# Kernel optimization log

Measured on AMD Instinct MI355X. Metric: run time of the kernel, lower is better.

## Reference

```python
import jax, jax.numpy as jnp
import numpy as np


def setup_inputs() -> dict:
    key = jax.random.key(0)
    x = jax.random.normal(key, (16, 2048, 512), dtype=jnp.float32)
    return {"x": x}


def reference(x):
    # Cosine (L2-normalized) self-attention.
    # norm: [B, N, 1] L2 norm over feature dim
    norm = jnp.sqrt(jnp.sum(x * x, axis=2, keepdims=True))
    # scores[b, i, j] = <x_i, x_j> / (|x_i| |x_j|)  -> [B, N, N]
    scores = jnp.einsum('bnd,bmd->bnm', x, x) / (norm * jnp.swapaxes(norm, -2, -1))
    p_attn = jax.nn.softmax(scores, axis=-1)
    # output: [B, N, D]
    return jnp.einsum('bnm,bmd->bnd', p_attn, x)
```

## Files before the change

kernel.cpp:

```cpp
#include <hip/hip_runtime.h>
#include <hip/hip_bf16.h>
#include <cstdint>
#include <cstddef>

#define BB 16
#define NN 2048
#define DD 512

typedef _Float16 f16x8 __attribute__((ext_vector_type(8)));
typedef _Float16 f16x4 __attribute__((ext_vector_type(4)));
typedef float f32x4 __attribute__((ext_vector_type(4)));

__device__ __forceinline__ void async_ld16(void* lds, const void* g) {
    __builtin_amdgcn_global_load_lds(
        (const __attribute__((address_space(1))) unsigned int*)(uintptr_t)g,
        (__attribute__((address_space(3))) unsigned int*)(uint32_t)(uintptr_t)lds,
        16, 0, 0);
}

#define VM_WAIT(n) asm volatile("s_waitcnt vmcnt(" #n ")" ::: "memory")
#define RAW_BAR()  do { asm volatile("" ::: "memory"); __builtin_amdgcn_s_barrier(); asm volatile("" ::: "memory"); } while (0)
#define LGKM_BAR() do { asm volatile("s_waitcnt lgkmcnt(0)" ::: "memory"); \
                        __builtin_amdgcn_s_barrier();                      \
                        __builtin_amdgcn_sched_barrier(0); } while (0)

__global__ __launch_bounds__(256) void k_prep(const float* __restrict__ x,
                                              _Float16* __restrict__ xhn,
                                              _Float16* __restrict__ vT,
                                              float* __restrict__ denom) {
    __shared__ _Float16 t[512 * 66];
    const int tid = threadIdx.x, lane = tid & 63, w = tid >> 6;
    const int b = blockIdx.y, j0 = blockIdx.x * 64;
    if (tid < 64) denom[b * NN + j0 + tid] = 0.f;
    const float* xb = x + ((size_t)b * NN + j0) * DD;

    for (int rr = 0; rr < 16; ++rr) {
        const int jj = w * 16 + rr;
        const float* xr = xb + (size_t)jj * DD;
        float4 a = ((const float4*)xr)[lane];
        float4 c = ((const float4*)xr)[lane + 64];
        float ss = a.x*a.x + a.y*a.y + a.z*a.z + a.w*a.w
                 + c.x*c.x + c.y*c.y + c.z*c.z + c.w*c.w;
        #pragma unroll
        for (int o = 1; o < 64; o <<= 1) ss += __shfl_xor(ss, o);
        const float rn = 1.0f / sqrtf(ss);
        _Float16* dst = xhn + ((size_t)b * NN + j0 + jj) * DD;
        f16x4 v0 = {(_Float16)(a.x*rn), (_Float16)(a.y*rn), (_Float16)(a.z*rn), (_Float16)(a.w*rn)};
        f16x4 v1 = {(_Float16)(c.x*rn), (_Float16)(c.y*rn), (_Float16)(c.z*rn), (_Float16)(c.w*rn)};
        *(f16x4*)(dst + 4 * lane) = v0;
        *(f16x4*)(dst + 256 + 4 * lane) = v1;
        const int d0 = 4 * lane, d1 = 256 + 4 * lane;
        t[(d0 + 0) * 66 + jj] = (_Float16)a.x;
        t[(d0 + 1) * 66 + jj] = (_Float16)a.y;
        t[(d0 + 2) * 66 + jj] = (_Float16)a.z;
        t[(d0 + 3) * 66 + jj] = (_Float16)a.w;
        t[(d1 + 0) * 66 + jj] = (_Float16)c.x;
        t[(d1 + 1) * 66 + jj] = (_Float16)c.y;
        t[(d1 + 2) * 66 + jj] = (_Float16)c.z;
        t[(d1 + 3) * 66 + jj] = (_Float16)c.w;
    }
    LGKM_BAR();
    #pragma unroll
    for (int it = 0; it < 16; ++it) {
        const int id = it * 256 + tid;
        const int d = id >> 3, ch = (id & 7) * 8;
        const uint32_t* tp = (const uint32_t*)&t[d * 66 + ch];
        uint4 v = {tp[0], tp[1], tp[2], tp[3]};
        *(uint4*)(vT + ((size_t)b * DD + d) * NN + j0 + ch) = v;
    }
}

__global__ __launch_bounds__(256) void k_scores(const _Float16* __restrict__ xhn,
                                                _Float16* __restrict__ W,
                                                float* __restrict__ denom) {
    __shared__ _Float16 smem[32768];
    const int tid = threadIdx.x;
    const int lane = tid & 63, wv = tid >> 6;
    const int wr = wv >> 1, wc = wv & 1;
    const int m_ = lane & 15, quad = lane >> 4;
    const int b = blockIdx.z;

    const int swz = (blockIdx.x % 8) * 17 + blockIdx.x / 8;
    int rem = swz, ti = 0, rowlen = NN / 128;
    while (rem >= rowlen) { rem -= rowlen; ++ti; --rowlen; }
    const int tj = ti + rem;
    const int I = ti * 128, J = tj * 128;
    const bool diag = (ti == tj);

    const _Float16* Ab = xhn + ((size_t)b * NN + I) * DD;
    const _Float16* Bb = xhn + ((size_t)b * NN + J) * DD;

    f32x4 acc[4][4];
    #pragma unroll
    for (int i = 0; i < 4; ++i)
        #pragma unroll
        for (int j = 0; j < 4; ++j) acc[i][j] = (f32x4){0.f, 0.f, 0.f, 0.f};

    const int sub = lane >> 3;
    const int swc = (lane & 7) ^ sub;
    const _Float16* agl = Ab + (size_t)(wv * 32 + sub) * DD + swc * 8;
    const _Float16* bgl = Bb + (size_t)(wv * 32 + sub) * DD + swc * 8;

#define S_STAGE(kb_) do {                                                     \
    _Float16* A_ = smem + (((kb_) & 1) << 14);                                \
    const int k0_ = (kb_) * 64;                                               \
    _Pragma("unroll")                                                         \
    for (int c = 0; c < 4; ++c) {                                             \
        async_ld16(&A_[(wv * 32 + c * 8) * 64], agl + (size_t)c * 8 * DD + k0_); \
        async_ld16(&A_[8192 + (wv * 32 + c * 8) * 64], bgl + (size_t)c * 8 * DD + k0_); \
    } } while (0)

#define S_COMPUTE(kb_) do {                                                   \
    const _Float16* As_ = smem + (((kb_) & 1) << 14);                         \
    const _Float16* Bs_ = As_ + 8192;                                         \
    _Pragma("unroll")                                                         \
    for (int kc = 0; kc < 2; ++kc) {                                          \
        f16x8 af[4], bf[4];                                                   \
        _Pragma("unroll")                                                     \
        for (int t = 0; t < 4; ++t) {                                         \
            const int Ra = wr * 64 + t * 16 + m_;                             \
            const int Rb = wc * 64 + t * 16 + m_;                             \
            af[t] = *(const f16x8*)&As_[Ra * 64 + (((kc * 4 + quad) ^ (Ra & 7)) * 8)]; \
            bf[t] = *(const f16x8*)&Bs_[Rb * 64 + (((kc * 4 + quad) ^ (Rb & 7)) * 8)]; \
        }                                                                     \
        _Pragma("unroll")                                                     \
        for (int i = 0; i < 4; ++i)                                           \
            _Pragma("unroll")                                                 \
            for (int j = 0; j < 4; ++j)                                       \
                acc[i][j] = __builtin_amdgcn_mfma_f32_16x16x32_f16(af[i], bf[j], acc[i][j], 0, 0, 0); \
    } } while (0)

    S_STAGE(0); S_STAGE(1);
    for (int kb = 0; kb < DD / 64 - 1; ++kb) {
        VM_WAIT(8);
        RAW_BAR();
        __builtin_amdgcn_s_setprio(1);
        S_COMPUTE(kb);
        __builtin_amdgcn_s_setprio(0);
        RAW_BAR();
        if (kb + 2 < DD / 64) S_STAGE(kb + 2);
    }
    VM_WAIT(0);
    RAW_BAR();
    __builtin_amdgcn_s_setprio(1);
    S_COMPUTE(DD / 64 - 1);
    __builtin_amdgcn_s_setprio(0);

    f16x4 wq[4][4];
    float rowpart[4][4];
    float colpart[4] = {0.f, 0.f, 0.f, 0.f};
    #pragma unroll
    for (int i = 0; i < 4; ++i)
        #pragma unroll
        for (int r = 0; r < 4; ++r) rowpart[i][r] = 0.f;

    #pragma unroll
    for (int i = 0; i < 4; ++i) {
        #pragma unroll
        for (int j = 0; j < 4; ++j) {
            #pragma unroll
            for (int r = 0; r < 4; ++r) {
                const float w = __expf(acc[i][j][r]);
                wq[i][j][r] = (_Float16)w;
                rowpart[i][r] += w;
                colpart[j] += w;
            }
        }
    }

    #pragma unroll
    for (int i = 0; i < 4; ++i) {
        #pragma unroll
        for (int r = 0; r < 4; ++r) {
            float s = rowpart[i][r];
            s += __shfl_xor(s, 1);
            s += __shfl_xor(s, 2);
            s += __shfl_xor(s, 4);
            s += __shfl_xor(s, 8);
            if (m_ == 0)
                atomicAdd(&denom[b * NN + I + wr * 64 + i * 16 + quad * 4 + r], s);
        }
    }
    if (!diag) {
        #pragma unroll
        for (int j = 0; j < 4; ++j) {
            float s = colpart[j];
            s += __shfl_xor(s, 16);
            s += __shfl_xor(s, 32);
            if (quad == 0)
                atomicAdd(&denom[b * NN + J + wc * 64 + j * 16 + m_], s);
        }
    }

    LGKM_BAR();

    _Float16* WtT = smem;
    #pragma unroll
    for (int i = 0; i < 4; ++i) {
        const int rowb = wr * 64 + i * 16 + quad * 4;
        #pragma unroll
        for (int j = 0; j < 4; ++j) {
            const int col = wc * 64 + j * 16 + m_;
            *(f16x4*)&WtT[col * 136 + rowb] = wq[i][j];
        }
    }
    LGKM_BAR();
    {
        const int rr = tid >> 1, off = (tid & 1) * 64;
        _Float16* wg = W + ((size_t)b * NN + J + rr) * NN + I + off;
        const _Float16* wl = &WtT[rr * 136 + off];
        #pragma unroll
        for (int c = 0; c < 64; c += 8)
            *(uint4*)(wg + c) = *(const uint4*)(wl + c);
    }
    if (!diag) {
        LGKM_BAR();
        _Float16* Wt = smem;
        #pragma unroll
        for (int i = 0; i < 4; ++i) {
            const int rowb = wr * 64 + i * 16 + quad * 4;
            #pragma unroll
            for (int j = 0; j < 4; ++j) {
                const int col = wc * 64 + j * 16 + m_;
                #pragma unroll
                for (int r = 0; r < 4; ++r)
                    Wt[(rowb + r) * 136 + col] = wq[i][j][r];
            }
        }
        LGKM_BAR();
        const int rr = tid >> 1, off = (tid & 1) * 64;
        _Float16* wg = W + ((size_t)b * NN + I + rr) * NN + J + off;
        const _Float16* wl = &Wt[rr * 136 + off];
        #pragma unroll
        for (int c = 0; c < 64; c += 8)
            *(uint4*)(wg + c) = *(const uint4*)(wl + c);
    }
#undef S_STAGE
#undef S_COMPUTE
}

__global__ __launch_bounds__(512, 2) void k_pv(const _Float16* __restrict__ W,
                                               const _Float16* __restrict__ vT,
                                               const float* __restrict__ denom,
                                               float* __restrict__ out) {
    extern __shared__ _Float16 smem[];
    float* rdI = (float*)(smem + 65536);
    const int tid = threadIdx.x;
    const int lane = tid & 63, w = tid >> 6;
    const int wr = w >> 2, wcol = w & 3;
    const int m_ = lane & 15, quad = lane >> 4;
    const int b = blockIdx.z;
    const int D0 = (blockIdx.x >> 3) * 256;
    const int I  = (blockIdx.x & 7) * 256;
    const _Float16* Ab = W  + ((size_t)b * NN + I) * NN;
    const _Float16* Bb = vT + ((size_t)b * DD + D0) * NN;

    const int sub = lane >> 3;
    const int swc = (lane & 7) ^ sub;
    const _Float16* agl = Ab + (size_t)(w * 32 + sub) * NN + swc * 8;
    const _Float16* bgl = Bb + (size_t)(w * 32 + sub) * NN + swc * 8;

    f32x4 acc[8][4];
    #pragma unroll
    for (int i = 0; i < 8; ++i)
        #pragma unroll
        for (int j = 0; j < 4; ++j) acc[i][j] = (f32x4){0.f, 0.f, 0.f, 0.f};

#define P_STAGE(kb_) do {                                                     \
    _Float16* A_ = smem + (((kb_) & 1) << 15);                                \
    const int k0_ = (kb_) * 64;                                               \
    _Pragma("unroll")                                                         \
    for (int c = 0; c < 4; ++c) {                                             \
        async_ld16(&A_[(w * 32 + c * 8) * 64], agl + (size_t)c * 8 * NN + k0_); \
        async_ld16(&A_[16384 + (w * 32 + c * 8) * 64], bgl + (size_t)c * 8 * NN + k0_); \
    } } while (0)

#define P_COMPUTE(kb_) do {                                                   \
    const _Float16* As_ = smem + (((kb_) & 1) << 15);                         \
    const _Float16* Bs_ = As_ + 16384;                                        \
    _Pragma("unroll")                                                         \
    for (int kc = 0; kc < 2; ++kc) {                                          \
        f16x8 af[8], bf[4];                                                   \
        _Pragma("unroll")                                                     \
        for (int i = 0; i < 8; ++i) {                                         \
            const int R = wr * 128 + i * 16 + m_;                             \
            af[i] = *(const f16x8*)&As_[R * 64 + (((kc * 4 + quad) ^ (R & 7)) * 8)]; \
        }                                                                     \
        _Pragma("unroll")                                                     \
        for (int j = 0; j < 4; ++j) {                                         \
            const int Rb = wcol * 64 + j * 16 + m_;                           \
            bf[j] = *(const f16x8*)&Bs_[Rb * 64 + (((kc * 4 + quad) ^ (Rb & 7)) * 8)]; \
        }                                                                     \
        _Pragma("unroll")                                                     \
        for (int i = 0; i < 8; ++i)                                           \
            _Pragma("unroll")                                                 \
            for (int j = 0; j < 4; ++j)                                       \
                acc[i][j] = __builtin_amdgcn_mfma_f32_16x16x32_f16(af[i], bf[j], acc[i][j], 0, 0, 0); \
    } } while (0)

    P_STAGE(0); P_STAGE(1);
    for (int kb = 0; kb < NN / 64 - 1; ++kb) {
        VM_WAIT(8);
        RAW_BAR();
        __builtin_amdgcn_s_setprio(1);
        P_COMPUTE(kb);
        __builtin_amdgcn_s_setprio(0);
        RAW_BAR();
        if (kb + 2 < NN / 64) P_STAGE(kb + 2);
    }
    VM_WAIT(0);
    RAW_BAR();
    __builtin_amdgcn_s_setprio(1);
    P_COMPUTE(NN / 64 - 1);
    __builtin_amdgcn_s_setprio(0);

    if (tid < 256) rdI[tid] = 1.0f / denom[b * NN + I + tid];
    LGKM_BAR();

    #pragma unroll
    for (int i = 0; i < 8; ++i) {
        const int rowb = wr * 128 + i * 16 + quad * 4;
        #pragma unroll
        for (int r = 0; r < 4; ++r) {
            const float sc = rdI[rowb + r];
            float* op = out + ((size_t)(b * NN + I + rowb + r)) * DD + D0;
            #pragma unroll
            for (int j = 0; j < 4; ++j)
                op[wcol * 64 + j * 16 + m_] = acc[i][j][r] * sc;
        }
    }
#undef P_STAGE
#undef P_COMPUTE
}

extern "C" void kernel_launch(void* const* d_in, const int* in_sizes, int n_in,
                              void* d_out, int out_size, void* d_ws, size_t ws_size,
                              hipStream_t stream) {
    const float* x = (const float*)d_in[0];
    char* ws = (char*)d_ws;
    _Float16* xhn   = (_Float16*)(ws);
    _Float16* vT    = (_Float16*)(ws + (size_t)33554432);
    _Float16* W     = (_Float16*)(ws + (size_t)67108864);
    float*    denom = (float*)   (ws + (size_t)201326592);
    float*    out   = (float*)d_out;

    k_prep<<<dim3(NN / 64, BB), 256, 0, stream>>>(x, xhn, vT, denom);
    const int npairs = (NN / 128) * (NN / 128 + 1) / 2;
    k_scores<<<dim3(npairs, 1, BB), 256, 0, stream>>>(xhn, W, denom);
    k_pv<<<dim3(16, 1, BB), 512, 132096, stream>>>(W, vT, denom, out);
}
```

Measured before the change: 208.2 us.

## Enlarge scores tile to 256x256 with 512 threads and flatten batch grid

```diff
diff --git a/kernel.cpp b/kernel.cpp
--- a/kernel.cpp
+++ b/kernel.cpp
@@ -70,61 +70,64 @@
     }
 }
 
-__global__ __launch_bounds__(256) void k_scores(const _Float16* __restrict__ xhn,
-                                                _Float16* __restrict__ W,
-                                                float* __restrict__ denom) {
-    __shared__ _Float16 smem[32768];
+__global__ __launch_bounds__(512, 2) void k_scores(const _Float16* __restrict__ xhn,
+                                                   _Float16* __restrict__ W,
+                                                   float* __restrict__ denom) {
+    extern __shared__ _Float16 smem[];
     const int tid = threadIdx.x;
-    const int lane = tid & 63, wv = tid >> 6;
-    const int wr = wv >> 1, wc = wv & 1;
+    const int lane = tid & 63, w = tid >> 6;
+    const int wr = w >> 2, wcol = w & 3;
     const int m_ = lane & 15, quad = lane >> 4;
-    const int b = blockIdx.z;
-
-    const int swz = (blockIdx.x % 8) * 17 + blockIdx.x / 8;
-    int rem = swz, ti = 0, rowlen = NN / 128;
+
+    const int swz = ((int)blockIdx.x % 8) * 72 + (int)blockIdx.x / 8;
+    const int b = swz / 36;
+    int rem = swz % 36, ti = 0, rowlen = NN / 256;
     while (rem >= rowlen) { rem -= rowlen; ++ti; --rowlen; }
     const int tj = ti + rem;
-    const int I = ti * 128, J = tj * 128;
+    const int I = ti * 256, J = tj * 256;
     const bool diag = (ti == tj);
 
     const _Float16* Ab = xhn + ((size_t)b * NN + I) * DD;
     const _Float16* Bb = xhn + ((size_t)b * NN + J) * DD;
 
-    f32x4 acc[4][4];
-    #pragma unroll
-    for (int i = 0; i < 4; ++i)
-        #pragma unroll
-        for (int j = 0; j < 4; ++j) acc[i][j] = (f32x4){0.f, 0.f, 0.f, 0.f};
-
     const int sub = lane >> 3;
     const int swc = (lane & 7) ^ sub;
-    const _Float16* agl = Ab + (size_t)(wv * 32 + sub) * DD + swc * 8;
-    const _Float16* bgl = Bb + (size_t)(wv * 32 + sub) * DD + swc * 8;
+    const _Float16* agl = Ab + (size_t)(w * 32 + sub) * DD + swc * 8;
+    const _Float16* bgl = Bb + (size_t)(w * 32 + sub) * DD + swc * 8;
+
+    f32x4 acc[8][4];
+    #pragma unroll
+    for (int i = 0; i < 8; ++i)
+        #pragma unroll
+        for (int j = 0; j < 4; ++j) acc[i][j] = (f32x4){0.f, 0.f, 0.f, 0.f};
 
 #define S_STAGE(kb_) do {                                                     \
-    _Float16* A_ = smem + (((kb_) & 1) << 14);                                \
+    _Float16* A_ = smem + (((kb_) & 1) << 15);                                \
     const int k0_ = (kb_) * 64;                                               \
     _Pragma("unroll")                                                         \
     for (int c = 0; c < 4; ++c) {                                             \
-        async_ld16(&A_[(wv * 32 + c * 8) * 64], agl + (size_t)c * 8 * DD + k0_); \
-        async_ld16(&A_[8192 + (wv * 32 + c * 8) * 64], bgl + (size_t)c * 8 * DD + k0_); \
+        async_ld16(&A_[(w * 32 + c * 8) * 64], agl + (size_t)c * 8 * DD + k0_); \
+        async_ld16(&A_[16384 + (w * 32 + c * 8) * 64], bgl + (size_t)c * 8 * DD + k0_); \
     } } while (0)
 
 #define S_COMPUTE(kb_) do {                                                   \
-    const _Float16* As_ = smem + (((kb_) & 1) << 14);                         \
-    const _Float16* Bs_ = As_ + 8192;                                         \
+    const _Float16* As_ = smem + (((kb_) & 1) << 15);                         \
+    const _Float16* Bs_ = As_ + 16384;                                        \
     _Pragma("unroll")                                                         \
     for (int kc = 0; kc < 2; ++kc) {                                          \
-        f16x8 af[4], bf[4];                                                   \
-        _Pragma("unroll")                                                     \
-        for (int t = 0; t < 4; ++t) {                                         \
-            const int Ra = wr * 64 + t * 16 + m_;                             \
-            const int Rb = wc * 64 + t * 16 + m_;                             \
-            af[t] = *(const f16x8*)&As_[Ra * 64 + (((kc * 4 + quad) ^ (Ra & 7)) * 8)]; \
-            bf[t] = *(const f16x8*)&Bs_[Rb * 64 + (((kc * 4 + quad) ^ (Rb & 7)) * 8)]; \
+        f16x8 af[8], bf[4];                                                   \
+        _Pragma("unroll")                                                     \
+        for (int i = 0; i < 8; ++i) {                                         \
+            const int R = wr * 128 + i * 16 + m_;                             \
+            af[i] = *(const f16x8*)&As_[R * 64 + (((kc * 4 + quad) ^ (R & 7)) * 8)]; \
         }                                                                     \
         _Pragma("unroll")                                                     \
-        for (int i = 0; i < 4; ++i)                                           \
+        for (int j = 0; j < 4; ++j) {                                         \
+            const int Rb = wcol * 64 + j * 16 + m_;                           \
+            bf[j] = *(const f16x8*)&Bs_[Rb * 64 + (((kc * 4 + quad) ^ (Rb & 7)) * 8)]; \
+        }                                                                     \
+        _Pragma("unroll")                                                     \
+        for (int i = 0; i < 8; ++i)                                           \
             _Pragma("unroll")                                                 \
             for (int j = 0; j < 4; ++j)                                       \
                 acc[i][j] = __builtin_amdgcn_mfma_f32_16x16x32_f16(af[i], bf[j], acc[i][j], 0, 0, 0); \
@@ -146,39 +149,30 @@
     S_COMPUTE(DD / 64 - 1);
     __builtin_amdgcn_s_setprio(0);
 
-    f16x4 wq[4][4];
-    float rowpart[4][4];
+    f16x4 wq[8][4];
     float colpart[4] = {0.f, 0.f, 0.f, 0.f};
     #pragma unroll
-    for (int i = 0; i < 4; ++i)
-        #pragma unroll
-        for (int r = 0; r < 4; ++r) rowpart[i][r] = 0.f;
-
-    #pragma unroll
-    for (int i = 0; i < 4; ++i) {
+    for (int i = 0; i < 8; ++i) {
+        float rp[4] = {0.f, 0.f, 0.f, 0.f};
         #pragma unroll
         for (int j = 0; j < 4; ++j) {
             #pragma unroll
             for (int r = 0; r < 4; ++r) {
-                const float w = __expf(acc[i][j][r]);
-                wq[i][j][r] = (_Float16)w;
-                rowpart[i][r] += w;
-                colpart[j] += w;
+                const float wv_ = __expf(acc[i][j][r]);
+                wq[i][j][r] = (_Float16)wv_;
+                rp[r] += wv_;
+                colpart[j] += wv_;
             }
         }
-    }
-
-    #pragma unroll
-    for (int i = 0; i < 4; ++i) {
         #pragma unroll
         for (int r = 0; r < 4; ++r) {
-            float s = rowpart[i][r];
+            float s = rp[r];
             s += __shfl_xor(s, 1);
             s += __shfl_xor(s, 2);
             s += __shfl_xor(s, 4);
             s += __shfl_xor(s, 8);
             if (m_ == 0)
-                atomicAdd(&denom[b * NN + I + wr * 64 + i * 16 + quad * 4 + r], s);
+                atomicAdd(&denom[b * NN + I + wr * 128 + i * 16 + quad * 4 + r], s);
         }
     }
     if (!diag) {
@@ -188,7 +182,7 @@
             s += __shfl_xor(s, 16);
             s += __shfl_xor(s, 32);
             if (quad == 0)
-                atomicAdd(&denom[b * NN + J + wc * 64 + j * 16 + m_], s);
+                atomicAdd(&denom[b * NN + J + wcol * 64 + j * 16 + m_], s);
         }
     }
 
@@ -196,44 +190,58 @@
 
     _Float16* WtT = smem;
     #pragma unroll
-    for (int i = 0; i < 4; ++i) {
-        const int rowb = wr * 64 + i * 16 + quad * 4;
-        #pragma unroll
-        for (int j = 0; j < 4; ++j) {
-            const int col = wc * 64 + j * 16 + m_;
-            *(f16x4*)&WtT[col * 136 + rowb] = wq[i][j];
-        }
-    }
-    LGKM_BAR();
-    {
-        const int rr = tid >> 1, off = (tid & 1) * 64;
-        _Float16* wg = W + ((size_t)b * NN + J + rr) * NN + I + off;
-        const _Float16* wl = &WtT[rr * 136 + off];
-        #pragma unroll
-        for (int c = 0; c < 64; c += 8)
-            *(uint4*)(wg + c) = *(const uint4*)(wl + c);
-    }
+    for (int s = 0; s < 2; ++s) {
+        if ((wcol >> 1) == s) {
+            #pragma unroll
+            for (int i = 0; i < 8; ++i) {
+                const int rowb = wr * 128 + i * 16 + quad * 4;
+                #pragma unroll
+                for (int j = 0; j < 4; ++j) {
+                    const int lc = (wcol & 1) * 64 + j * 16 + m_;
+                    *(f16x4*)&WtT[lc * 264 + rowb] = wq[i][j];
+                }
+            }
+        }
+        LGKM_BAR();
+        {
+            const int rr = tid >> 2, off = (tid & 3) * 64;
+            _Float16* wg = W + ((size_t)b * NN + J + s * 128 + rr) * NN + I + off;
+            const _Float16* wl = &WtT[rr * 264 + off];
+            #pragma unroll
+            for (int c = 0; c < 64; c += 8)
+                *(uint4*)(wg + c) = *(const uint4*)(wl + c);
+        }
+        LGKM_BAR();
+    }
+
     if (!diag) {
-        LGKM_BAR();
         _Float16* Wt = smem;
         #pragma unroll
-        for (int i = 0; i < 4; ++i) {
-            const int rowb = wr * 64 + i * 16 + quad * 4;
-            #pragma unroll
-            for (int j = 0; j < 4; ++j) {
-                const int col = wc * 64 + j * 16 + m_;
+        for (int s = 0; s < 2; ++s) {
+            if (wr == s) {
                 #pragma unroll
-                for (int r = 0; r < 4; ++r)
-                    Wt[(rowb + r) * 136 + col] = wq[i][j][r];
+                for (int i = 0; i < 8; ++i) {
+                    const int lr0 = i * 16 + quad * 4;
+                    #pragma unroll
+                    for (int j = 0; j < 4; ++j) {
+                        const int col = wcol * 64 + j * 16 + m_;
+                        #pragma unroll
+                        for (int r = 0; r < 4; ++r)
+                            Wt[(lr0 + r) * 264 + col] = wq[i][j][r];
+                    }
+                }
             }
-        }
-        LGKM_BAR();
-        const int rr = tid >> 1, off = (tid & 1) * 64;
-        _Float16* wg = W + ((size_t)b * NN + I + rr) * NN + J + off;
-        const _Float16* wl = &Wt[rr * 136 + off];
-        #pragma unroll
-        for (int c = 0; c < 64; c += 8)
-            *(uint4*)(wg + c) = *(const uint4*)(wl + c);
+            LGKM_BAR();
+            {
+                const int rr = tid >> 2, off = (tid & 3) * 64;
+                _Float16* wg = W + ((size_t)b * NN + I + s * 128 + rr) * NN + J + off;
+                const _Float16* wl = &Wt[rr * 264 + off];
+                #pragma unroll
+                for (int c = 0; c < 64; c += 8)
+                    *(uint4*)(wg + c) = *(const uint4*)(wl + c);
+            }
+            LGKM_BAR();
+        }
     }
 #undef S_STAGE
 #undef S_COMPUTE
@@ -345,7 +353,7 @@
     float*    out   = (float*)d_out;
 
     k_prep<<<dim3(NN / 64, BB), 256, 0, stream>>>(x, xhn, vT, denom);
-    const int npairs = (NN / 128) * (NN / 128 + 1) / 2;
-    k_scores<<<dim3(npairs, 1, BB), 256, 0, stream>>>(xhn, W, denom);
+    const int npairs16 = (NN / 256) * (NN / 256 + 1) / 2 * BB;
+    k_scores<<<dim3(npairs16, 1, 1), 512, 131072, stream>>>(xhn, W, denom);
     k_pv<<<dim3(16, 1, BB), 512, 132096, stream>>>(W, vT, denom, out);
 }
```

New measurement: 210.5 us. Within noise of the previous version (+1.1%).

## Split PV k-tile compute into four barrier-separated quadrants with interleaved LDS loads

Applied to the files above, without the earlier changes.

```diff
diff --git a/kernel.cpp b/kernel.cpp
--- a/kernel.cpp
+++ b/kernel.cpp
@@ -23,6 +23,8 @@
 #define LGKM_BAR() do { asm volatile("s_waitcnt lgkmcnt(0)" ::: "memory"); \
                         __builtin_amdgcn_s_barrier();                      \
                         __builtin_amdgcn_sched_barrier(0); } while (0)
+#define LGKM0_FENCE() do { asm volatile("s_waitcnt lgkmcnt(0)" ::: "memory"); \
+                           __builtin_amdgcn_sched_barrier(0); } while (0)
 
 __global__ __launch_bounds__(256) void k_prep(const float* __restrict__ x,
                                               _Float16* __restrict__ xhn,
@@ -266,6 +268,9 @@
         #pragma unroll
         for (int j = 0; j < 4; ++j) acc[i][j] = (f32x4){0.f, 0.f, 0.f, 0.f};
 
+    f16x8 afq[4][2];
+    f16x8 bfq[4][2];
+
 #define P_STAGE(kb_) do {                                                     \
     _Float16* A_ = smem + (((kb_) & 1) << 15);                                \
     const int k0_ = (kb_) * 64;                                               \
@@ -275,44 +280,62 @@
         async_ld16(&A_[16384 + (w * 32 + c * 8) * 64], bgl + (size_t)c * 8 * NN + k0_); \
     } } while (0)
 
-#define P_COMPUTE(kb_) do {                                                   \
-    const _Float16* As_ = smem + (((kb_) & 1) << 15);                         \
-    const _Float16* Bs_ = As_ + 16384;                                        \
+#define LD_A(t_, ih_) do {                                                    \
+    const int R = wr * 128 + ((ih_) * 4 + (t_)) * 16 + m_;                    \
+    afq[t_][0] = *(const f16x8*)&As_[R * 64 + ((quad ^ (R & 7)) * 8)];        \
+    afq[t_][1] = *(const f16x8*)&As_[R * 64 + (((4 + quad) ^ (R & 7)) * 8)];  \
+    } while (0)
+
+#define LD_B(j_) do {                                                         \
+    const int Rb = wcol * 64 + (j_) * 16 + m_;                                \
+    bfq[j_][0] = *(const f16x8*)&Bs_[Rb * 64 + ((quad ^ (Rb & 7)) * 8)];      \
+    bfq[j_][1] = *(const f16x8*)&Bs_[Rb * 64 + (((4 + quad) ^ (Rb & 7)) * 8)];\
+    } while (0)
+
+#define MFMA_Q(ih_, jh_) do {                                                 \
+    __builtin_amdgcn_s_setprio(1);                                            \
     _Pragma("unroll")                                                         \
-    for (int kc = 0; kc < 2; ++kc) {                                          \
-        f16x8 af[8], bf[4];                                                   \
+    for (int t = 0; t < 4; ++t)                                               \
         _Pragma("unroll")                                                     \
-        for (int i = 0; i < 8; ++i) {                                         \
-            const int R = wr * 128 + i * 16 + m_;                             \
-            af[i] = *(const f16x8*)&As_[R * 64 + (((kc * 4 + quad) ^ (R & 7)) * 8)]; \
+        for (int j = 0; j < 2; ++j) {                                         \
+            acc[(ih_)*4+t][(jh_)*2+j] = __builtin_amdgcn_mfma_f32_16x16x32_f16( \
+                afq[t][0], bfq[(jh_)*2+j][0], acc[(ih_)*4+t][(jh_)*2+j], 0, 0, 0); \
+            acc[(ih_)*4+t][(jh_)*2+j] = __builtin_amdgcn_mfma_f32_16x16x32_f16( \
+                afq[t][1], bfq[(jh_)*2+j][1], acc[(ih_)*4+t][(jh_)*2+j], 0, 0, 0); \
         }                                                                     \
-        _Pragma("unroll")                                                     \
-        for (int j = 0; j < 4; ++j) {                                         \
-            const int Rb = wcol * 64 + j * 16 + m_;                           \
-            bf[j] = *(const f16x8*)&Bs_[Rb * 64 + (((kc * 4 + quad) ^ (Rb & 7)) * 8)]; \
-        }                                                                     \
-        _Pragma("unroll")                                                     \
-        for (int i = 0; i < 8; ++i)                                           \
-            _Pragma("unroll")                                                 \
-            for (int j = 0; j < 4; ++j)                                       \
-                acc[i][j] = __builtin_amdgcn_mfma_f32_16x16x32_f16(af[i], bf[j], acc[i][j], 0, 0, 0); \
-    } } while (0)
+    __builtin_amdgcn_s_setprio(0);                                            \
+    } while (0)
 
     P_STAGE(0); P_STAGE(1);
-    for (int kb = 0; kb < NN / 64 - 1; ++kb) {
-        VM_WAIT(8);
-        RAW_BAR();
-        __builtin_amdgcn_s_setprio(1);
-        P_COMPUTE(kb);
-        __builtin_amdgcn_s_setprio(0);
-        RAW_BAR();
-        if (kb + 2 < NN / 64) P_STAGE(kb + 2);
-    }
-    VM_WAIT(0);
-    RAW_BAR();
-    __builtin_amdgcn_s_setprio(1);
-    P_COMPUTE(NN / 64 - 1);
-    __builtin_amdgcn_s_setprio(0);
+    const int NT = NN / 64;
+    for (int tc = 0; tc < NT; ++tc) {
+        const _Float16* As_ = smem + ((tc & 1) << 15);
+        const _Float16* Bs_ = As_ + 16384;
+        if (tc == NT - 1) { VM_WAIT(0); } else { VM_WAIT(8); }
+        RAW_BAR();
+        #pragma unroll
+        for (int t = 0; t < 4; ++t) LD_A(t, 0);
+        LD_B(0); LD_B(1);
+        RAW_BAR();
+        LGKM0_FENCE();
+        MFMA_Q(0, 0);
+        RAW_BAR();
+        LD_B(2); LD_B(3);
+        RAW_BAR();
+        LGKM0_FENCE();
+        MFMA_Q(0, 1);
+        RAW_BAR();
+        #pragma unroll
+        for (int t = 0; t < 4; ++t) LD_A(t, 1);
+        RAW_BAR();
+        LGKM0_FENCE();
+        MFMA_Q(1, 0);
+        RAW_BAR();
+        if (tc + 2 < NT) P_STAGE(tc + 2);
+        RAW_BAR();
+        MFMA_Q(1, 1);
+        RAW_BAR();
+    }
 
     if (tid < 256) rdI[tid] = 1.0f / denom[b * NN + I + tid];
     LGKM_BAR();
@@ -330,7 +353,9 @@
         }
     }
 #undef P_STAGE
-#undef P_COMPUTE
+#undef LD_A
+#undef LD_B
+#undef MFMA_Q
 }
 
 extern "C" void kernel_launch(void* const* d_in, const int* in_sizes, int n_in,
```

Measured after the change: 207.3 us. No clear change (-0.4%).
